# Performance work log

Measured on AMD Instinct MI355X. Metric: run time of the kernel, lower is better.

## Reference

```python
import jax, jax.numpy as jnp
import numpy as np
from jax import lax

B, T, DIN, D = 8, 4096, 1024, 256
H, DK, DV, DFF, P = 8, 32, 32, 1024, 4
KC, NS = 64, 4
SCALES = jnp.array([16.0, 64.0, 128.0, 256.0], dtype=jnp.float32)
K = KC * NS


def _pos_embedding(rel, d_model):
    # rel: [B,K,2] normalized (start,end) -> sinusoidal emb [B,K,d_model]
    d4 = d_model // 4
    freq = jnp.exp(-jnp.log(10000.0) * jnp.arange(d4, dtype=jnp.float32) / d4)
    ang = rel[..., None] * freq                                  # [B,K,2,d4]
    emb = jnp.concatenate([jnp.sin(ang), jnp.cos(ang)], axis=-1) # [B,K,2,2*d4]
    return emb.reshape(rel.shape[0], rel.shape[1], d_model)


def _pool(feat, s, e):
    # ROI pooling by P linearly spaced samples in [s,e); feat [B,T,D], s/e [B,K]
    frac = (jnp.arange(P, dtype=jnp.float32) + 0.5) / P
    idx = jnp.clip(jnp.floor(s[..., None] + (e - s)[..., None] * frac), 0, T - 1).astype(jnp.int32)
    b, k = idx.shape[0], idx.shape[1]
    out = jnp.take_along_axis(feat, idx.reshape(b, k * P)[..., None], axis=1)  # [B,K*P,D]
    return out.reshape(b, k, P, feat.shape[-1])


def _ln(x, g, b):
    m = x.mean(-1, keepdims=True)
    v = ((x - m) ** 2).mean(-1, keepdims=True)
    return (x - m) * lax.rsqrt(v + 1e-6) * g + b


def setup_inputs():
    ks = jax.random.split(jax.random.key(0), 16)
    n = lambda i, sh, s=0.02: jax.random.normal(ks[i], sh, jnp.float32) * s
    return dict(
        feature=jax.random.normal(ks[0], (B, T, DIN), jnp.float32),
        pos_ind=jnp.tile(jnp.arange(T, dtype=jnp.int32)[None], (B, 1)),
        feature_mask=jnp.ones((B, T), jnp.float32),
        W_red=n(1, (DIN, D)), b_red=jnp.zeros((D,), jnp.float32),
        conv1_w=n(2, (D, D, 3)), conv1_b=jnp.zeros((D,), jnp.float32),
        conv2_w=n(3, (D, D, 3)), conv2_b=jnp.zeros((D,), jnp.float32),
        W_sc=n(4, (D, 3)), b_sc=jnp.zeros((3,), jnp.float32),
        W_pool=n(5, (3 * P * D, D)), b_pool=jnp.zeros((D,), jnp.float32),
        Wq=n(6, (D, H * DK)), Wk=n(7, (D, H * DK)), Wv=n(8, (D, H * DV)),
        Wo=n(9, (H * DV, D)),
        ln1_g=jnp.ones((D,), jnp.float32), ln1_b=jnp.zeros((D,), jnp.float32),
        W1=n(10, (D, DFF)), b1=jnp.zeros((DFF,), jnp.float32),
        W2=n(11, (DFF, D)), b2=jnp.zeros((D,), jnp.float32),
        ln2_g=jnp.ones((D,), jnp.float32), ln2_b=jnp.zeros((D,), jnp.float32),
        W_cls=n(12, (D, 2)), b_cls=jnp.zeros((2,), jnp.float32),
    )


def _forward(feature, feature_mask, W_red, b_red, conv1_w, conv1_b, conv2_w, conv2_b,
             W_sc, b_sc, W_pool, b_pool, Wq, Wk, Wv, Wo, ln1_g, ln1_b,
             W1, b1, W2, b2, ln2_g, ln2_b, W_cls, b_cls):
    enc_input = jax.nn.selu(feature @ W_red + b_red)            # [B,T,D]
    h = enc_input.transpose(0, 2, 1)                            # [B,D,T]
    dn = ('NCH', 'OIH', 'NCH')
    h = jax.nn.relu(lax.conv_general_dilated(h, conv1_w, (1,), [(1, 1)], dimension_numbers=dn) + conv1_b[None, :, None])
    h = jax.nn.relu(lax.conv_general_dilated(h, conv2_w, (1,), [(1, 1)], dimension_numbers=dn) + conv2_b[None, :, None])
    enc_output = h.transpose(0, 2, 1)                           # [B,T,D]
    score_output = jax.nn.sigmoid(enc_output @ W_sc + b_sc)     # [B,T,3]

    # --- proposal_layer (fixed-size, jit-safe): top-KC actness peaks x NS scales ---
    actness = score_output[..., 0] * feature_mask               # [B,T]
    topv, topi = lax.top_k(actness, KC)                         # [B,KC]
    c = topi.astype(jnp.float32)[:, :, None]                    # [B,KC,1]
    half = SCALES[None, None, :] / 2.0
    s = jnp.clip(c - half, 0.0, T - 1.0).reshape(B, K)
    e = jnp.clip(c + half, 1.0, float(T)).reshape(B, K)
    e = jnp.maximum(e, s + 1.0)
    L = e - s
    ss, se = jnp.clip(s - L / 4, 0.0, T - 1.0), s + L / 4       # start region
    es, ee = e - L / 4, jnp.clip(e + L / 4, 1.0, float(T))      # end region
    rois_mask = jnp.broadcast_to((topv > 0.5)[:, :, None], (B, KC, NS)).reshape(B, K).astype(jnp.float32)
    roi_actness = jnp.broadcast_to(topv[:, :, None], (B, KC, NS)).reshape(B, K)
    rel = jnp.stack([s / T, e / T], axis=-1)                    # [B,K,2]
    pos_emb = _pos_embedding(rel, D)                            # [B,K,D]

    # --- ROI_Relation: pool(start/mid/end) -> fc -> MHSA + FFN (post-LN) ---
    pooled = jnp.concatenate([_pool(enc_input, ss, se), _pool(enc_input, s, e), _pool(enc_input, es, ee)], axis=2)
    x0 = pooled.reshape(B, K, 3 * P * D) @ W_pool + b_pool + pos_emb  # [B,K,D]
    q = (x0 @ Wq).reshape(B, K, H, DK)
    kk = (x0 @ Wk).reshape(B, K, H, DK)
    v = (x0 @ Wv).reshape(B, K, H, DV)
    att = jnp.einsum('bqhd,bkhd->bhqk', q, kk) / np.sqrt(DK).astype(np.float32)
    att = att + (1.0 - rois_mask)[:, None, None, :] * -1e9
    ctx = jnp.einsum('bhqk,bkhd->bqhd', jax.nn.softmax(att, axis=-1), v).reshape(B, K, H * DV)
    x1 = _ln(x0 + ctx @ Wo, ln1_g, ln1_b)
    x2 = _ln(x1 + jax.nn.relu(x1 @ W1 + b1) @ W2 + b2, ln2_g, ln2_b)
    roi_scores = jax.nn.softmax(x2 @ W_cls + b_cls, axis=2)     # [B,K,2]
    rois_se = jnp.stack([s, e], axis=-1)                        # rois[:, :, 1:]
    return rois_se, roi_actness, roi_scores


def reference(feature, pos_ind, feature_mask, W_red, b_red, conv1_w, conv1_b, conv2_w, conv2_b, W_sc, b_sc, W_pool, b_pool, Wq, Wk, Wv, Wo, ln1_g, ln1_b, W1, b1, W2, b2, ln2_g, ln2_b, W_cls, b_cls):
    del pos_ind  # carried through pipeline but unused in this forward
    return _forward(feature, feature_mask, W_red, b_red, conv1_w, conv1_b, conv2_w, conv2_b, W_sc, b_sc, W_pool, b_pool, Wq, Wk, Wv, Wo, ln1_g, ln1_b, W1, b1, W2, b2, ln2_g, ln2_b, W_cls, b_cls)
```

## Files before the change

### kernel.cpp

```cpp
#include <hip/hip_runtime.h>
#include <hip/hip_bf16.h>
#include <math.h>

#define NB 8
#define NT 4096
#define NBT 32768
#define NDIN 1024
#define ND 256
#define NH 8
#define NDK 32
#define NKC 64
#define NNS 4
#define NRK 256
#define NROI 2048

#define F4Z make_float4(0.f, 0.f, 0.f, 0.f)

__global__ __launch_bounds__(256) void transw_k(const float* __restrict__ w1,
    const float* __restrict__ w2, float* __restrict__ Wt1, float* __restrict__ Wt2)
{
  int i = blockIdx.x * 256 + threadIdx.x;
  const float* w = (i >= 196608) ? w2 : w1;
  float* Wt = (i >= 196608) ? Wt2 : Wt1;
  int j = (i >= 196608) ? (i - 196608) : i;
  int co = j & 255;
  int rest = j >> 8;
  int ci = rest & 255;
  int tap = rest >> 8;
  Wt[j] = w[(size_t)co * 768 + ci * 3 + tap];
}

__global__ __launch_bounds__(256) void gemm1_k(const float* __restrict__ A,
    const float* __restrict__ W, const float* __restrict__ bias,
    float* __restrict__ C, int M, int Ka, int N)
{
  __shared__ float As[16][132];
  __shared__ float Ws[16][128];
  int tid = threadIdx.x;
  int tx = tid & 15, ty = tid >> 4;
  int m0 = blockIdx.x * 128, n0 = blockIdx.y * 128;
  int ar = tid >> 1, acg = tid & 1;
  int wk = tid >> 5, wn = tid & 31;
  float acc[8][8] = {};
  for (int kk = 0; kk < Ka; kk += 16) {
#pragma unroll
    for (int p = 0; p < 2; ++p) {
      int cg = acg * 2 + p;
      float4 av = *reinterpret_cast<const float4*>(A + (size_t)(m0 + ar) * Ka + kk + cg * 4);
      As[cg * 4 + 0][ar] = av.x;
      As[cg * 4 + 1][ar] = av.y;
      As[cg * 4 + 2][ar] = av.z;
      As[cg * 4 + 3][ar] = av.w;
    }
#pragma unroll
    for (int p = 0; p < 2; ++p) {
      int k = wk + p * 8;
      *reinterpret_cast<float4*>(&Ws[k][wn * 4]) =
          *reinterpret_cast<const float4*>(W + (size_t)(kk + k) * N + n0 + wn * 4);
    }
    __syncthreads();
#pragma unroll
    for (int k = 0; k < 16; ++k) {
      float4 xa = *reinterpret_cast<const float4*>(&As[k][ty * 4]);
      float4 xb = *reinterpret_cast<const float4*>(&As[k][64 + ty * 4]);
      float4 wa = *reinterpret_cast<const float4*>(&Ws[k][tx * 4]);
      float4 wb = *reinterpret_cast<const float4*>(&Ws[k][64 + tx * 4]);
      float aa[8] = {xa.x, xa.y, xa.z, xa.w, xb.x, xb.y, xb.z, xb.w};
      float bb[8] = {wa.x, wa.y, wa.z, wa.w, wb.x, wb.y, wb.z, wb.w};
#pragma unroll
      for (int i = 0; i < 8; ++i)
#pragma unroll
        for (int j = 0; j < 8; ++j)
          acc[i][j] += aa[i] * bb[j];
    }
    __syncthreads();
  }
#pragma unroll
  for (int i = 0; i < 8; ++i) {
    int row = m0 + ((i < 4) ? (ty * 4 + i) : (64 + ty * 4 + (i - 4)));
#pragma unroll
    for (int jh = 0; jh < 2; ++jh) {
      int col = n0 + jh * 64 + tx * 4;
      float o[4];
#pragma unroll
      for (int j = 0; j < 4; ++j) {
        float v = acc[i][jh * 4 + j] + bias[col + j];
        v = (v > 0.f) ? 1.0507009873554805f * v
                      : 1.0507009873554805f * 1.6732632423543772f * expm1f(v);
        o[j] = v;
      }
      *reinterpret_cast<float4*>(C + (size_t)row * N + col) =
          make_float4(o[0], o[1], o[2], o[3]);
    }
  }
}

template<int EPI>
__global__ __launch_bounds__(256) void conv_t(const float* __restrict__ in,
    const float* __restrict__ Wt, const float* __restrict__ bias,
    float* __restrict__ out, const float* __restrict__ Wsc,
    float* __restrict__ pscore)
{
  __shared__ float As[16][132];
  __shared__ float Ws[16][128];
  int tid = threadIdx.x;
  int tx = tid & 15, ty = tid >> 4;
  int m0 = blockIdx.x * 128, n0 = blockIdx.y * 128;
  int bstart = m0 & ~(NT - 1);
  int ar = tid >> 1, acg = tid & 1;
  int wk = tid >> 5, wn = tid & 31;
  float acc[8][8] = {};
  for (int kk = 0; kk < 768; kk += 16) {
    int tap = kk >> 8, kd = kk & 255;
    int g = m0 - 1 + tap + ar;
    bool ok = (g >= bstart) && (g < bstart + NT);
#pragma unroll
    for (int p = 0; p < 2; ++p) {
      int cg = acg * 2 + p;
      float4 av = ok ? *reinterpret_cast<const float4*>(in + (size_t)g * 256 + kd + cg * 4)
                     : F4Z;
      As[cg * 4 + 0][ar] = av.x;
      As[cg * 4 + 1][ar] = av.y;
      As[cg * 4 + 2][ar] = av.z;
      As[cg * 4 + 3][ar] = av.w;
    }
#pragma unroll
    for (int p = 0; p < 2; ++p) {
      int k = wk + p * 8;
      *reinterpret_cast<float4*>(&Ws[k][wn * 4]) =
          *reinterpret_cast<const float4*>(Wt + (size_t)(kk + k) * 256 + n0 + wn * 4);
    }
    __syncthreads();
#pragma unroll
    for (int k = 0; k < 16; ++k) {
      float4 xa = *reinterpret_cast<const float4*>(&As[k][ty * 4]);
      float4 xb = *reinterpret_cast<const float4*>(&As[k][64 + ty * 4]);
      float4 wa = *reinterpret_cast<const float4*>(&Ws[k][tx * 4]);
      float4 wb = *reinterpret_cast<const float4*>(&Ws[k][64 + tx * 4]);
      float aa[8] = {xa.x, xa.y, xa.z, xa.w, xb.x, xb.y, xb.z, xb.w};
      float bb[8] = {wa.x, wa.y, wa.z, wa.w, wb.x, wb.y, wb.z, wb.w};
#pragma unroll
      for (int i = 0; i < 8; ++i)
#pragma unroll
        for (int j = 0; j < 8; ++j)
          acc[i][j] += aa[i] * bb[j];
    }
    __syncthreads();
  }

  if (EPI == 0) {
#pragma unroll
    for (int i = 0; i < 8; ++i) {
      int row = m0 + ((i < 4) ? (ty * 4 + i) : (64 + ty * 4 + (i - 4)));
#pragma unroll
      for (int jh = 0; jh < 2; ++jh) {
        int col = n0 + jh * 64 + tx * 4;
        float o[4];
#pragma unroll
        for (int j = 0; j < 4; ++j)
          o[j] = fmaxf(acc[i][jh * 4 + j] + bias[col + j], 0.f);
        *reinterpret_cast<float4*>(out + (size_t)row * 256 + col) =
            make_float4(o[0], o[1], o[2], o[3]);
      }
    }
  } else {
    float p[8];
#pragma unroll
    for (int i = 0; i < 8; ++i) {
      float s = 0.f;
#pragma unroll
      for (int jh = 0; jh < 2; ++jh)
#pragma unroll
        for (int j = 0; j < 4; ++j) {
          int col = n0 + jh * 64 + tx * 4 + j;
          float v = fmaxf(acc[i][jh * 4 + j] + bias[col], 0.f);
          s += v * Wsc[col * 3];
        }
      p[i] = s;
    }
#pragma unroll
    for (int off = 1; off < 16; off <<= 1)
#pragma unroll
      for (int i = 0; i < 8; ++i)
        p[i] += __shfl_xor(p[i], off, 64);
    if (tx == 0) {
#pragma unroll
      for (int i = 0; i < 8; ++i) {
        int row = m0 + ((i < 4) ? (ty * 4 + i) : (64 + ty * 4 + (i - 4)));
        pscore[(size_t)row * 2 + blockIdx.y] = p[i];
      }
    }
  }
}

__global__ __launch_bounds__(256) void actness_k(const float* __restrict__ pscore,
    const float* __restrict__ bsc, const float* __restrict__ fmask,
    float* __restrict__ actness)
{
  int g = blockIdx.x * 256 + threadIdx.x;
  float2 pv = *reinterpret_cast<const float2*>(pscore + (size_t)g * 2);
  float z = pv.x + pv.y + bsc[0];
  actness[g] = (1.f / (1.f + expf(-z))) * fmask[g];
}

template<int ACT>
__global__ __launch_bounds__(256) void gemm_k(const float* __restrict__ A,
    const float* __restrict__ W, const float* __restrict__ bias,
    const float* __restrict__ resid, float* __restrict__ C,
    int M, int Ka, int N)
{
  __shared__ float As[16][66];
  __shared__ float Ws[16][68];
  int tid = threadIdx.x;
  int tx = tid & 15, ty = tid >> 4;
  int m0 = blockIdx.x * 64, n0 = blockIdx.y * 64;
  int lr = tid >> 2, lc = tid & 3;
  int wr = tid >> 4, wc = tid & 15;
  float acc[4][4] = {};
  for (int kk = 0; kk < Ka; kk += 16) {
    float4 av = *reinterpret_cast<const float4*>(A + (size_t)(m0 + lr) * Ka + kk + lc * 4);
    As[lc * 4 + 0][lr] = av.x;
    As[lc * 4 + 1][lr] = av.y;
    As[lc * 4 + 2][lr] = av.z;
    As[lc * 4 + 3][lr] = av.w;
    float4 wv = *reinterpret_cast<const float4*>(W + (size_t)(kk + wr) * N + n0 + wc * 4);
    *reinterpret_cast<float4*>(&Ws[wr][wc * 4]) = wv;
    __syncthreads();
#pragma unroll
    for (int k = 0; k < 16; ++k) {
      float4 a4 = *reinterpret_cast<const float4*>(&As[k][ty * 4]);
      float4 b4 = *reinterpret_cast<const float4*>(&Ws[k][tx * 4]);
      float aa[4] = {a4.x, a4.y, a4.z, a4.w};
      float bb[4] = {b4.x, b4.y, b4.z, b4.w};
#pragma unroll
      for (int i = 0; i < 4; ++i)
#pragma unroll
        for (int j = 0; j < 4; ++j)
          acc[i][j] += aa[i] * bb[j];
    }
    __syncthreads();
  }
#pragma unroll
  for (int i = 0; i < 4; ++i) {
    int row = m0 + ty * 4 + i;
    float o[4];
#pragma unroll
    for (int j = 0; j < 4; ++j) {
      int col = n0 + tx * 4 + j;
      float v = acc[i][j];
      if (bias) v += bias[col];
      if (resid) v += resid[(size_t)row * N + col];
      if (ACT == 1) {
        v = (v > 0.f) ? 1.0507009873554805f * v
                      : 1.0507009873554805f * 1.6732632423543772f * expm1f(v);
      } else if (ACT == 2) {
        v = fmaxf(v, 0.f);
      }
      o[j] = v;
    }
    *reinterpret_cast<float4*>(C + (size_t)row * N + n0 + tx * 4) =
        make_float4(o[0], o[1], o[2], o[3]);
  }
}

__global__ __launch_bounds__(256) void topk_k(const float* __restrict__ actness,
    float* __restrict__ topv, int* __restrict__ topi)
{
  __shared__ float wbv[4];
  __shared__ int wbi[4];
  __shared__ float gbv;
  __shared__ int gbi;
  int b = blockIdx.x;
  int tid = threadIdx.x;
  int lane = tid & 63, wvi = tid >> 6;
  float v[16];
  const float* src = actness + (size_t)b * NT + tid * 16;
#pragma unroll
  for (int j = 0; j < 16; j += 4)
    *reinterpret_cast<float4*>(&v[j]) = *reinterpret_cast<const float4*>(src + j);
  for (int it = 0; it < NKC; ++it) {
    float best = -1e30f; int bj = 0;
#pragma unroll
    for (int j = 0; j < 16; ++j)
      if (v[j] > best) { best = v[j]; bj = j; }
    int bidx = tid * 16 + bj;
#pragma unroll
    for (int off = 1; off < 64; off <<= 1) {
      float ov = __shfl_xor(best, off, 64);
      int oi = __shfl_xor(bidx, off, 64);
      if (ov > best || (ov == best && oi < bidx)) { best = ov; bidx = oi; }
    }
    if (lane == 0) { wbv[wvi] = best; wbi[wvi] = bidx; }
    __syncthreads();
    if (tid == 0) {
      float bb = wbv[0]; int bi2 = wbi[0];
#pragma unroll
      for (int w = 1; w < 4; ++w)
        if (wbv[w] > bb || (wbv[w] == bb && wbi[w] < bi2)) { bb = wbv[w]; bi2 = wbi[w]; }
      topv[b * NKC + it] = bb;
      topi[b * NKC + it] = bi2;
      gbv = bb; gbi = bi2;
    }
    __syncthreads();
    int gi = gbi;
    if ((gi >> 4) == tid) v[gi & 15] = -1e30f;
  }
}

__global__ __launch_bounds__(256) void rois_k(const float* __restrict__ topv,
    const int* __restrict__ topi, int* __restrict__ idxb, float* __restrict__ rmask,
    float* __restrict__ rel, float* __restrict__ out_rois, float* __restrict__ out_act)
{
  int t = blockIdx.x * 256 + threadIdx.x;
  if (t >= NROI) return;
  int b = t >> 8, k = t & 255, kc = k >> 2, ns = k & 3;
  float tv = topv[b * NKC + kc];
  float c = (float)topi[b * NKC + kc];
  const float scales[4] = {16.f, 64.f, 128.f, 256.f};
  float half = scales[ns] * 0.5f;
  float s = fminf(fmaxf(c - half, 0.f), 4095.f);
  float e = fminf(fmaxf(c + half, 1.f), 4096.f);
  e = fmaxf(e, s + 1.f);
  float L = e - s;
  float ss = fminf(fmaxf(s - L * 0.25f, 0.f), 4095.f);
  float se = s + L * 0.25f;
  float es = e - L * 0.25f;
  float ee = fminf(fmaxf(e + L * 0.25f, 1.f), 4096.f);
  float st[3] = {ss, s, es};
  float en[3] = {se, e, ee};
#pragma unroll
  for (int r = 0; r < 3; ++r)
#pragma unroll
    for (int p = 0; p < 4; ++p) {
      float frac = ((float)p + 0.5f) * 0.25f;
      float fidx = floorf(st[r] + (en[r] - st[r]) * frac);
      fidx = fminf(fmaxf(fidx, 0.f), 4095.f);
      idxb[t * 12 + r * 4 + p] = (int)fidx;
    }
  rmask[t] = (tv > 0.5f) ? 1.f : 0.f;
  rel[t * 2 + 0] = s * (1.f / 4096.f);
  rel[t * 2 + 1] = e * (1.f / 4096.f);
  out_rois[t * 2 + 0] = s;
  out_rois[t * 2 + 1] = e;
  out_act[t] = tv;
}

__global__ __launch_bounds__(256) void pool_gemm_k(const float* __restrict__ enc,
    const int* __restrict__ idxb, const float* __restrict__ Wp,
    const float* __restrict__ bp, const float* __restrict__ rel,
    float* __restrict__ x0)
{
  __shared__ float As[16][66];
  __shared__ float Ws[16][68];
  int tid = threadIdx.x;
  int tx = tid & 15, ty = tid >> 4;
  int m0 = blockIdx.x * 64, n0 = blockIdx.y * 64;
  int lr = tid >> 2, lc = tid & 3;
  int wr = tid >> 4, wc = tid & 15;
  int roi = m0 + lr;
  int b = roi >> 8;
  float acc[4][4] = {};
  for (int kk = 0; kk < 3072; kk += 16) {
    int slot = kk >> 8, kd = kk & 255;
    int trow = idxb[roi * 12 + slot];
    float4 av = *reinterpret_cast<const float4*>(
        enc + ((size_t)(b * NT + trow)) * 256 + kd + lc * 4);
    As[lc * 4 + 0][lr] = av.x;
    As[lc * 4 + 1][lr] = av.y;
    As[lc * 4 + 2][lr] = av.z;
    As[lc * 4 + 3][lr] = av.w;
    float4 wv = *reinterpret_cast<const float4*>(Wp + (size_t)(kk + wr) * 256 + n0 + wc * 4);
    *reinterpret_cast<float4*>(&Ws[wr][wc * 4]) = wv;
    __syncthreads();
#pragma unroll
    for (int k = 0; k < 16; ++k) {
      float4 a4 = *reinterpret_cast<const float4*>(&As[k][ty * 4]);
      float4 b4 = *reinterpret_cast<const float4*>(&Ws[k][tx * 4]);
      float aa[4] = {a4.x, a4.y, a4.z, a4.w};
      float bb[4] = {b4.x, b4.y, b4.z, b4.w};
#pragma unroll
      for (int i = 0; i < 4; ++i)
#pragma unroll
        for (int j = 0; j < 4; ++j)
          acc[i][j] += aa[i] * bb[j];
    }
    __syncthreads();
  }
#pragma unroll
  for (int i = 0; i < 4; ++i) {
    int rr = m0 + ty * 4 + i;
    float r0 = rel[rr * 2], r1 = rel[rr * 2 + 1];
    float o[4];
#pragma unroll
    for (int j = 0; j < 4; ++j) {
      int col = n0 + tx * 4 + j;
      int rsel = col >> 7, cc = col & 127, j2 = cc & 63;
      float freq = expf(-0.14391156831212787f * (float)j2);
      float ang = ((rsel == 0) ? r0 : r1) * freq;
      float pe = (cc < 64) ? sinf(ang) : cosf(ang);
      o[j] = acc[i][j] + bp[col] + pe;
    }
    *reinterpret_cast<float4*>(x0 + (size_t)rr * 256 + n0 + tx * 4) =
        make_float4(o[0], o[1], o[2], o[3]);
  }
}

__global__ __launch_bounds__(256) void attn_k(const float* __restrict__ q,
    const float* __restrict__ kbuf, const float* __restrict__ vbuf,
    const float* __restrict__ rmask, float* __restrict__ ctx)
{
  __shared__ float ks[256][32];
  __shared__ float vs[256][32];
  int bh = blockIdx.x;
  int b = bh >> 3, h = bh & 7;
  int tid = threadIdx.x;
  size_t base = ((size_t)b * 256) * 256 + h * 32;
  for (int idx = tid; idx < 2048; idx += 256) {
    int r = idx >> 3, dg = idx & 7;
    *reinterpret_cast<float4*>(&ks[r][dg * 4]) =
        *reinterpret_cast<const float4*>(kbuf + base + (size_t)r * 256 + dg * 4);
    *reinterpret_cast<float4*>(&vs[r][dg * 4]) =
        *reinterpret_cast<const float4*>(vbuf + base + (size_t)r * 256 + dg * 4);
  }
  __syncthreads();
  float qr[32];
#pragma unroll
  for (int dg = 0; dg < 8; ++dg)
    *reinterpret_cast<float4*>(&qr[dg * 4]) =
        *reinterpret_cast<const float4*>(q + base + (size_t)tid * 256 + dg * 4);
  const float invs = 0.17677669529663689f;
  float m = -1e30f;
  for (int kk = 0; kk < 256; ++kk) {
    float s = 0.f;
#pragma unroll
    for (int d = 0; d < 32; ++d) s += qr[d] * ks[kk][d];
    s = s * invs + (1.f - rmask[b * 256 + kk]) * -1e9f;
    m = fmaxf(m, s);
  }
  float l = 0.f;
  float accd[32] = {};
  for (int kk = 0; kk < 256; ++kk) {
    float s = 0.f;
#pragma unroll
    for (int d = 0; d < 32; ++d) s += qr[d] * ks[kk][d];
    s = s * invs + (1.f - rmask[b * 256 + kk]) * -1e9f;
    float p = expf(s - m);
    l += p;
#pragma unroll
    for (int d = 0; d < 32; ++d) accd[d] += p * vs[kk][d];
  }
  float inv = 1.f / l;
#pragma unroll
  for (int dg = 0; dg < 8; ++dg) {
    float4 o = make_float4(accd[dg * 4] * inv, accd[dg * 4 + 1] * inv,
                           accd[dg * 4 + 2] * inv, accd[dg * 4 + 3] * inv);
    *reinterpret_cast<float4*>(ctx + base + (size_t)tid * 256 + dg * 4) = o;
  }
}

__global__ __launch_bounds__(256) void ln_k(float* __restrict__ x,
    const float* __restrict__ g, const float* __restrict__ bb)
{
  int row = blockIdx.x * 4 + (threadIdx.x >> 6);
  int lane = threadIdx.x & 63;
  float* xr = x + (size_t)row * 256;
  float4 v = *reinterpret_cast<const float4*>(xr + lane * 4);
  float s = v.x + v.y + v.z + v.w;
#pragma unroll
  for (int off = 32; off > 0; off >>= 1) s += __shfl_xor(s, off, 64);
  float mean = s * 0.00390625f;
  float dx[4] = {v.x - mean, v.y - mean, v.z - mean, v.w - mean};
  float s2 = dx[0] * dx[0] + dx[1] * dx[1] + dx[2] * dx[2] + dx[3] * dx[3];
#pragma unroll
  for (int off = 32; off > 0; off >>= 1) s2 += __shfl_xor(s2, off, 64);
  float var = s2 * 0.00390625f;
  float rs = 1.f / sqrtf(var + 1e-6f);
  int c = lane * 4;
  float4 o;
  o.x = dx[0] * rs * g[c + 0] + bb[c + 0];
  o.y = dx[1] * rs * g[c + 1] + bb[c + 1];
  o.z = dx[2] * rs * g[c + 2] + bb[c + 2];
  o.w = dx[3] * rs * g[c + 3] + bb[c + 3];
  *reinterpret_cast<float4*>(xr + lane * 4) = o;
}

__global__ __launch_bounds__(256) void cls_k(const float* __restrict__ x2,
    const float* __restrict__ Wc, const float* __restrict__ bc,
    float* __restrict__ out)
{
  int r = blockIdx.x * 256 + threadIdx.x;
  if (r >= NROI) return;
  float l0 = bc[0], l1 = bc[1];
  const float* xr = x2 + (size_t)r * 256;
  for (int c = 0; c < 256; ++c) {
    float xv = xr[c];
    l0 += xv * Wc[c * 2 + 0];
    l1 += xv * Wc[c * 2 + 1];
  }
  float mm = fmaxf(l0, l1);
  float e0 = expf(l0 - mm), e1 = expf(l1 - mm);
  float inv = 1.f / (e0 + e1);
  out[r * 2 + 0] = e0 * inv;
  out[r * 2 + 1] = e1 * inv;
}

extern "C" void kernel_launch(void* const* d_in, const int* in_sizes, int n_in,
                              void* d_out, int out_size, void* d_ws, size_t ws_size,
                              hipStream_t stream) {
  (void)in_sizes; (void)n_in; (void)out_size; (void)ws_size;
  const float* feature = (const float*)d_in[0];
  const float* fmask   = (const float*)d_in[2];
  const float* W_red   = (const float*)d_in[3];
  const float* b_red   = (const float*)d_in[4];
  const float* conv1_w = (const float*)d_in[5];
  const float* conv1_b = (const float*)d_in[6];
  const float* conv2_w = (const float*)d_in[7];
  const float* conv2_b = (const float*)d_in[8];
  const float* W_sc    = (const float*)d_in[9];
  const float* b_sc    = (const float*)d_in[10];
  const float* W_pool  = (const float*)d_in[11];
  const float* b_pool  = (const float*)d_in[12];
  const float* Wq      = (const float*)d_in[13];
  const float* Wk      = (const float*)d_in[14];
  const float* Wv      = (const float*)d_in[15];
  const float* Wo      = (const float*)d_in[16];
  const float* ln1_g   = (const float*)d_in[17];
  const float* ln1_b   = (const float*)d_in[18];
  const float* W1      = (const float*)d_in[19];
  const float* b1      = (const float*)d_in[20];
  const float* W2      = (const float*)d_in[21];
  const float* b2      = (const float*)d_in[22];
  const float* ln2_g   = (const float*)d_in[23];
  const float* ln2_b   = (const float*)d_in[24];
  const float* W_cls   = (const float*)d_in[25];
  const float* b_cls   = (const float*)d_in[26];

  float* ws = (float*)d_ws;
  float* enc   = ws;
  float* h1    = ws + 8388608;
  float* Wt1   = ws + 16777216;
  float* Wt2   = ws + 16973824;
  float* act   = ws + 17170432;
  float* topv  = ws + 17203200;
  int*   topi  = (int*)(ws + 17203712);
  int*   idxb  = (int*)(ws + 17204224);
  float* rmask = ws + 17228800;
  float* rel   = ws + 17230848;
  float* pscore = ws + 17234944;
  float* x0  = h1;
  float* qb  = h1 + 524288;
  float* kb  = h1 + 1048576;
  float* vb  = h1 + 1572864;
  float* ctx = h1 + 2097152;
  float* x1  = h1 + 2621440;
  float* ft  = h1 + 3145728;
  float* x2  = h1 + 5242880;

  float* orois  = (float*)d_out;
  float* oact   = orois + 4096;
  float* oscore = orois + 6144;

  transw_k<<<1536, 256, 0, stream>>>(conv1_w, conv2_w, Wt1, Wt2);
  gemm1_k<<<dim3(256, 2), 256, 0, stream>>>(feature, W_red, b_red, enc,
                                            NBT, NDIN, ND);
  conv_t<0><<<dim3(256, 2), 256, 0, stream>>>(enc, Wt1, conv1_b, h1, nullptr, nullptr);
  conv_t<1><<<dim3(256, 2), 256, 0, stream>>>(h1, Wt2, conv2_b, nullptr, W_sc, pscore);
  actness_k<<<128, 256, 0, stream>>>(pscore, b_sc, fmask, act);
  topk_k<<<NB, 256, 0, stream>>>(act, topv, topi);
  rois_k<<<NB, 256, 0, stream>>>(topv, topi, idxb, rmask, rel, orois, oact);
  pool_gemm_k<<<dim3(32, 4), 256, 0, stream>>>(enc, idxb, W_pool, b_pool, rel, x0);
  gemm_k<0><<<dim3(32, 4), 256, 0, stream>>>(x0, Wq, nullptr, nullptr, qb, NROI, ND, ND);
  gemm_k<0><<<dim3(32, 4), 256, 0, stream>>>(x0, Wk, nullptr, nullptr, kb, NROI, ND, ND);
  gemm_k<0><<<dim3(32, 4), 256, 0, stream>>>(x0, Wv, nullptr, nullptr, vb, NROI, ND, ND);
  attn_k<<<NB * NH, 256, 0, stream>>>(qb, kb, vb, rmask, ctx);
  gemm_k<0><<<dim3(32, 4), 256, 0, stream>>>(ctx, Wo, nullptr, x0, x1, NROI, ND, ND);
  ln_k<<<512, 256, 0, stream>>>(x1, ln1_g, ln1_b);
  gemm_k<2><<<dim3(32, 16), 256, 0, stream>>>(x1, W1, b1, nullptr, ft, NROI, ND, 1024);
  gemm_k<0><<<dim3(32, 4), 256, 0, stream>>>(ft, W2, b2, x1, x2, NROI, 1024, ND);
  ln_k<<<512, 256, 0, stream>>>(x2, ln2_g, ln2_b);
  cls_k<<<NB, 256, 0, stream>>>(x2, W_cls, b_cls, oscore);
}
```

Before: 1.116 ms.

## Register-prefetch GEMM tiles, fuse QKV projection, online-softmax attention, warp-parallel classifier

Adds register double-buffering to every tiled GEMM/conv kernel, so the next K-chunk's global loads are issued before the current chunk's FMAs. This is meant to hide load latency, at the cost of an extra barrier per iteration and more registers. It also concatenates Wq/Wk/Wv into one weight and runs a single QKV GEMM, which cuts launches and rereads of x0. Attention switches to a single-pass online softmax, and the classifier head uses one wavefront per ROI with shuffle reductions instead of a serial per-thread loop.

```diff
diff --git a/kernel.cpp b/kernel.cpp
--- a/kernel.cpp
+++ b/kernel.cpp
@@ -30,6 +30,17 @@
   Wt[j] = w[(size_t)co * 768 + ci * 3 + tap];
 }
 
+__global__ __launch_bounds__(256) void concatw_k(const float* __restrict__ Wq,
+    const float* __restrict__ Wk, const float* __restrict__ Wv,
+    float* __restrict__ Wqkv)
+{
+  int d = blockIdx.x * 256 + threadIdx.x;
+  int r = d / 768, c = d % 768;
+  int m = c >> 8, cc = c & 255;
+  const float* src = (m == 0) ? Wq : (m == 1) ? Wk : Wv;
+  Wqkv[d] = src[r * 256 + cc];
+}
+
 __global__ __launch_bounds__(256) void gemm1_k(const float* __restrict__ A,
     const float* __restrict__ W, const float* __restrict__ bias,
     float* __restrict__ C, int M, int Ka, int N)
@@ -41,24 +52,31 @@
   int m0 = blockIdx.x * 128, n0 = blockIdx.y * 128;
   int ar = tid >> 1, acg = tid & 1;
   int wk = tid >> 5, wn = tid & 31;
+  float4 pa0, pa1, pw0, pw1;
+
+#define G1LOAD(kk) do { \
+    pa0 = *reinterpret_cast<const float4*>(A + (size_t)(m0 + ar) * Ka + (kk) + (acg * 2 + 0) * 4); \
+    pa1 = *reinterpret_cast<const float4*>(A + (size_t)(m0 + ar) * Ka + (kk) + (acg * 2 + 1) * 4); \
+    pw0 = *reinterpret_cast<const float4*>(W + (size_t)((kk) + wk) * N + n0 + wn * 4); \
+    pw1 = *reinterpret_cast<const float4*>(W + (size_t)((kk) + 8 + wk) * N + n0 + wn * 4); \
+  } while (0)
+#define G1WRITE() do { \
+    int cg0 = acg * 2, cg1 = acg * 2 + 1; \
+    As[cg0 * 4 + 0][ar] = pa0.x; As[cg0 * 4 + 1][ar] = pa0.y; \
+    As[cg0 * 4 + 2][ar] = pa0.z; As[cg0 * 4 + 3][ar] = pa0.w; \
+    As[cg1 * 4 + 0][ar] = pa1.x; As[cg1 * 4 + 1][ar] = pa1.y; \
+    As[cg1 * 4 + 2][ar] = pa1.z; As[cg1 * 4 + 3][ar] = pa1.w; \
+    *reinterpret_cast<float4*>(&Ws[wk][wn * 4]) = pw0; \
+    *reinterpret_cast<float4*>(&Ws[8 + wk][wn * 4]) = pw1; \
+  } while (0)
+
+  int NC = Ka >> 4;
   float acc[8][8] = {};
-  for (int kk = 0; kk < Ka; kk += 16) {
-#pragma unroll
-    for (int p = 0; p < 2; ++p) {
-      int cg = acg * 2 + p;
-      float4 av = *reinterpret_cast<const float4*>(A + (size_t)(m0 + ar) * Ka + kk + cg * 4);
-      As[cg * 4 + 0][ar] = av.x;
-      As[cg * 4 + 1][ar] = av.y;
-      As[cg * 4 + 2][ar] = av.z;
-      As[cg * 4 + 3][ar] = av.w;
-    }
-#pragma unroll
-    for (int p = 0; p < 2; ++p) {
-      int k = wk + p * 8;
-      *reinterpret_cast<float4*>(&Ws[k][wn * 4]) =
-          *reinterpret_cast<const float4*>(W + (size_t)(kk + k) * N + n0 + wn * 4);
-    }
-    __syncthreads();
+  G1LOAD(0);
+  G1WRITE();
+  __syncthreads();
+  for (int c = 0; c < NC; ++c) {
+    if (c + 1 < NC) G1LOAD((c + 1) * 16);
 #pragma unroll
     for (int k = 0; k < 16; ++k) {
       float4 xa = *reinterpret_cast<const float4*>(&As[k][ty * 4]);
@@ -74,7 +92,13 @@
           acc[i][j] += aa[i] * bb[j];
     }
     __syncthreads();
-  }
+    if (c + 1 < NC) {
+      G1WRITE();
+      __syncthreads();
+    }
+  }
+#undef G1LOAD
+#undef G1WRITE
 #pragma unroll
   for (int i = 0; i < 8; ++i) {
     int row = m0 + ((i < 4) ? (ty * 4 + i) : (64 + ty * 4 + (i - 4)));
@@ -109,28 +133,33 @@
   int bstart = m0 & ~(NT - 1);
   int ar = tid >> 1, acg = tid & 1;
   int wk = tid >> 5, wn = tid & 31;
+  float4 pa0, pa1, pw0, pw1;
+
+#define CLOAD(kk) do { \
+    int tap = (kk) >> 8, kd = (kk) & 255; \
+    int g = m0 - 1 + tap + ar; \
+    bool ok = (g >= bstart) && (g < bstart + NT); \
+    pa0 = ok ? *reinterpret_cast<const float4*>(in + (size_t)g * 256 + kd + (acg * 2 + 0) * 4) : F4Z; \
+    pa1 = ok ? *reinterpret_cast<const float4*>(in + (size_t)g * 256 + kd + (acg * 2 + 1) * 4) : F4Z; \
+    pw0 = *reinterpret_cast<const float4*>(Wt + (size_t)((kk) + wk) * 256 + n0 + wn * 4); \
+    pw1 = *reinterpret_cast<const float4*>(Wt + (size_t)((kk) + 8 + wk) * 256 + n0 + wn * 4); \
+  } while (0)
+#define CWRITE() do { \
+    int cg0 = acg * 2, cg1 = acg * 2 + 1; \
+    As[cg0 * 4 + 0][ar] = pa0.x; As[cg0 * 4 + 1][ar] = pa0.y; \
+    As[cg0 * 4 + 2][ar] = pa0.z; As[cg0 * 4 + 3][ar] = pa0.w; \
+    As[cg1 * 4 + 0][ar] = pa1.x; As[cg1 * 4 + 1][ar] = pa1.y; \
+    As[cg1 * 4 + 2][ar] = pa1.z; As[cg1 * 4 + 3][ar] = pa1.w; \
+    *reinterpret_cast<float4*>(&Ws[wk][wn * 4]) = pw0; \
+    *reinterpret_cast<float4*>(&Ws[8 + wk][wn * 4]) = pw1; \
+  } while (0)
+
   float acc[8][8] = {};
-  for (int kk = 0; kk < 768; kk += 16) {
-    int tap = kk >> 8, kd = kk & 255;
-    int g = m0 - 1 + tap + ar;
-    bool ok = (g >= bstart) && (g < bstart + NT);
-#pragma unroll
-    for (int p = 0; p < 2; ++p) {
-      int cg = acg * 2 + p;
-      float4 av = ok ? *reinterpret_cast<const float4*>(in + (size_t)g * 256 + kd + cg * 4)
-                     : F4Z;
-      As[cg * 4 + 0][ar] = av.x;
-      As[cg * 4 + 1][ar] = av.y;
-      As[cg * 4 + 2][ar] = av.z;
-      As[cg * 4 + 3][ar] = av.w;
-    }
-#pragma unroll
-    for (int p = 0; p < 2; ++p) {
-      int k = wk + p * 8;
-      *reinterpret_cast<float4*>(&Ws[k][wn * 4]) =
-          *reinterpret_cast<const float4*>(Wt + (size_t)(kk + k) * 256 + n0 + wn * 4);
-    }
-    __syncthreads();
+  CLOAD(0);
+  CWRITE();
+  __syncthreads();
+  for (int c = 0; c < 48; ++c) {
+    if (c + 1 < 48) CLOAD((c + 1) * 16);
 #pragma unroll
     for (int k = 0; k < 16; ++k) {
       float4 xa = *reinterpret_cast<const float4*>(&As[k][ty * 4]);
@@ -146,7 +175,13 @@
           acc[i][j] += aa[i] * bb[j];
     }
     __syncthreads();
-  }
+    if (c + 1 < 48) {
+      CWRITE();
+      __syncthreads();
+    }
+  }
+#undef CLOAD
+#undef CWRITE
 
   if (EPI == 0) {
 #pragma unroll
@@ -216,16 +251,25 @@
   int m0 = blockIdx.x * 64, n0 = blockIdx.y * 64;
   int lr = tid >> 2, lc = tid & 3;
   int wr = tid >> 4, wc = tid & 15;
+  float4 pav, pwv;
+  int NC = Ka >> 4;
+
+#define GLOAD(kk) do { \
+    pav = *reinterpret_cast<const float4*>(A + (size_t)(m0 + lr) * Ka + (kk) + lc * 4); \
+    pwv = *reinterpret_cast<const float4*>(W + (size_t)((kk) + wr) * N + n0 + wc * 4); \
+  } while (0)
+#define GWRITE() do { \
+    As[lc * 4 + 0][lr] = pav.x; As[lc * 4 + 1][lr] = pav.y; \
+    As[lc * 4 + 2][lr] = pav.z; As[lc * 4 + 3][lr] = pav.w; \
+    *reinterpret_cast<float4*>(&Ws[wr][wc * 4]) = pwv; \
+  } while (0)
+
   float acc[4][4] = {};
-  for (int kk = 0; kk < Ka; kk += 16) {
-    float4 av = *reinterpret_cast<const float4*>(A + (size_t)(m0 + lr) * Ka + kk + lc * 4);
-    As[lc * 4 + 0][lr] = av.x;
-    As[lc * 4 + 1][lr] = av.y;
-    As[lc * 4 + 2][lr] = av.z;
-    As[lc * 4 + 3][lr] = av.w;
-    float4 wv = *reinterpret_cast<const float4*>(W + (size_t)(kk + wr) * N + n0 + wc * 4);
-    *reinterpret_cast<float4*>(&Ws[wr][wc * 4]) = wv;
-    __syncthreads();
+  GLOAD(0);
+  GWRITE();
+  __syncthreads();
+  for (int c = 0; c < NC; ++c) {
+    if (c + 1 < NC) GLOAD((c + 1) * 16);
 #pragma unroll
     for (int k = 0; k < 16; ++k) {
       float4 a4 = *reinterpret_cast<const float4*>(&As[k][ty * 4]);
@@ -239,7 +283,13 @@
           acc[i][j] += aa[i] * bb[j];
     }
     __syncthreads();
-  }
+    if (c + 1 < NC) {
+      GWRITE();
+      __syncthreads();
+    }
+  }
+#undef GLOAD
+#undef GWRITE
 #pragma unroll
   for (int i = 0; i < 4; ++i) {
     int row = m0 + ty * 4 + i;
@@ -359,19 +409,26 @@
   int wr = tid >> 4, wc = tid & 15;
   int roi = m0 + lr;
   int b = roi >> 8;
+  float4 pav, pwv;
+
+#define PLOAD(kk) do { \
+    int slot = (kk) >> 8, kd = (kk) & 255; \
+    int trow = idxb[roi * 12 + slot]; \
+    pav = *reinterpret_cast<const float4*>(enc + ((size_t)(b * NT + trow)) * 256 + kd + lc * 4); \
+    pwv = *reinterpret_cast<const float4*>(Wp + (size_t)((kk) + wr) * 256 + n0 + wc * 4); \
+  } while (0)
+#define PWRITE() do { \
+    As[lc * 4 + 0][lr] = pav.x; As[lc * 4 + 1][lr] = pav.y; \
+    As[lc * 4 + 2][lr] = pav.z; As[lc * 4 + 3][lr] = pav.w; \
+    *reinterpret_cast<float4*>(&Ws[wr][wc * 4]) = pwv; \
+  } while (0)
+
   float acc[4][4] = {};
-  for (int kk = 0; kk < 3072; kk += 16) {
-    int slot = kk >> 8, kd = kk & 255;
-    int trow = idxb[roi * 12 + slot];
-    float4 av = *reinterpret_cast<const float4*>(
-        enc + ((size_t)(b * NT + trow)) * 256 + kd + lc * 4);
-    As[lc * 4 + 0][lr] = av.x;
-    As[lc * 4 + 1][lr] = av.y;
-    As[lc * 4 + 2][lr] = av.z;
-    As[lc * 4 + 3][lr] = av.w;
-    float4 wv = *reinterpret_cast<const float4*>(Wp + (size_t)(kk + wr) * 256 + n0 + wc * 4);
-    *reinterpret_cast<float4*>(&Ws[wr][wc * 4]) = wv;
-    __syncthreads();
+  PLOAD(0);
+  PWRITE();
+  __syncthreads();
+  for (int c = 0; c < 192; ++c) {
+    if (c + 1 < 192) PLOAD((c + 1) * 16);
 #pragma unroll
     for (int k = 0; k < 16; ++k) {
       float4 a4 = *reinterpret_cast<const float4*>(&As[k][ty * 4]);
@@ -385,7 +442,13 @@
           acc[i][j] += aa[i] * bb[j];
     }
     __syncthreads();
-  }
+    if (c + 1 < 192) {
+      PWRITE();
+      __syncthreads();
+    }
+  }
+#undef PLOAD
+#undef PWRITE
 #pragma unroll
   for (int i = 0; i < 4; ++i) {
     int rr = m0 + ty * 4 + i;
@@ -405,8 +468,7 @@
   }
 }
 
-__global__ __launch_bounds__(256) void attn_k(const float* __restrict__ q,
-    const float* __restrict__ kbuf, const float* __restrict__ vbuf,
+__global__ __launch_bounds__(256) void attn_k(const float* __restrict__ qkv,
     const float* __restrict__ rmask, float* __restrict__ ctx)
 {
   __shared__ float ks[256][32];
@@ -414,36 +476,35 @@
   int bh = blockIdx.x;
   int b = bh >> 3, h = bh & 7;
   int tid = threadIdx.x;
-  size_t base = ((size_t)b * 256) * 256 + h * 32;
+  size_t rowb = (size_t)b * 256;
   for (int idx = tid; idx < 2048; idx += 256) {
     int r = idx >> 3, dg = idx & 7;
     *reinterpret_cast<float4*>(&ks[r][dg * 4]) =
-        *reinterpret_cast<const float4*>(kbuf + base + (size_t)r * 256 + dg * 4);
+        *reinterpret_cast<const float4*>(qkv + (rowb + r) * 768 + 256 + h * 32 + dg * 4);
     *reinterpret_cast<float4*>(&vs[r][dg * 4]) =
-        *reinterpret_cast<const float4*>(vbuf + base + (size_t)r * 256 + dg * 4);
+        *reinterpret_cast<const float4*>(qkv + (rowb + r) * 768 + 512 + h * 32 + dg * 4);
   }
   __syncthreads();
   float qr[32];
 #pragma unroll
   for (int dg = 0; dg < 8; ++dg)
     *reinterpret_cast<float4*>(&qr[dg * 4]) =
-        *reinterpret_cast<const float4*>(q + base + (size_t)tid * 256 + dg * 4);
+        *reinterpret_cast<const float4*>(qkv + (rowb + tid) * 768 + h * 32 + dg * 4);
   const float invs = 0.17677669529663689f;
-  float m = -1e30f;
-  for (int kk = 0; kk < 256; ++kk) {
-    float s = 0.f;
-#pragma unroll
-    for (int d = 0; d < 32; ++d) s += qr[d] * ks[kk][d];
-    s = s * invs + (1.f - rmask[b * 256 + kk]) * -1e9f;
-    m = fmaxf(m, s);
-  }
-  float l = 0.f;
+  float m = -1e30f, l = 0.f;
   float accd[32] = {};
   for (int kk = 0; kk < 256; ++kk) {
     float s = 0.f;
 #pragma unroll
     for (int d = 0; d < 32; ++d) s += qr[d] * ks[kk][d];
     s = s * invs + (1.f - rmask[b * 256 + kk]) * -1e9f;
+    if (s > m) {
+      float corr = expf(m - s);
+      l *= corr;
+#pragma unroll
+      for (int d = 0; d < 32; ++d) accd[d] *= corr;
+      m = s;
+    }
     float p = expf(s - m);
     l += p;
 #pragma unroll
@@ -454,7 +515,7 @@
   for (int dg = 0; dg < 8; ++dg) {
     float4 o = make_float4(accd[dg * 4] * inv, accd[dg * 4 + 1] * inv,
                            accd[dg * 4 + 2] * inv, accd[dg * 4 + 3] * inv);
-    *reinterpret_cast<float4*>(ctx + base + (size_t)tid * 256 + dg * 4) = o;
+    *reinterpret_cast<float4*>(ctx + (rowb + tid) * 256 + h * 32 + dg * 4) = o;
   }
 }
 
@@ -488,20 +549,28 @@
     const float* __restrict__ Wc, const float* __restrict__ bc,
     float* __restrict__ out)
 {
-  int r = blockIdx.x * 256 + threadIdx.x;
-  if (r >= NROI) return;
-  float l0 = bc[0], l1 = bc[1];
-  const float* xr = x2 + (size_t)r * 256;
-  for (int c = 0; c < 256; ++c) {
-    float xv = xr[c];
-    l0 += xv * Wc[c * 2 + 0];
-    l1 += xv * Wc[c * 2 + 1];
-  }
-  float mm = fmaxf(l0, l1);
-  float e0 = expf(l0 - mm), e1 = expf(l1 - mm);
-  float inv = 1.f / (e0 + e1);
-  out[r * 2 + 0] = e0 * inv;
-  out[r * 2 + 1] = e1 * inv;
+  int row = blockIdx.x * 4 + (threadIdx.x >> 6);
+  int lane = threadIdx.x & 63;
+  const float* xr = x2 + (size_t)row * 256;
+  float4 xv = *reinterpret_cast<const float4*>(xr + lane * 4);
+  int c = lane * 4;
+  float4 w01 = *reinterpret_cast<const float4*>(Wc + c * 2);
+  float4 w23 = *reinterpret_cast<const float4*>(Wc + c * 2 + 4);
+  float l0 = xv.x * w01.x + xv.y * w01.z + xv.z * w23.x + xv.w * w23.z;
+  float l1 = xv.x * w01.y + xv.y * w01.w + xv.z * w23.y + xv.w * w23.w;
+#pragma unroll
+  for (int off = 32; off > 0; off >>= 1) {
+    l0 += __shfl_xor(l0, off, 64);
+    l1 += __shfl_xor(l1, off, 64);
+  }
+  if (lane == 0) {
+    l0 += bc[0]; l1 += bc[1];
+    float mm = fmaxf(l0, l1);
+    float e0 = expf(l0 - mm), e1 = expf(l1 - mm);
+    float inv = 1.f / (e0 + e1);
+    out[row * 2 + 0] = e0 * inv;
+    out[row * 2 + 1] = e1 * inv;
+  }
 }
 
 extern "C" void kernel_launch(void* const* d_in, const int* in_sizes, int n_in,
@@ -547,14 +616,13 @@
   float* rmask = ws + 17228800;
   float* rel   = ws + 17230848;
   float* pscore = ws + 17234944;
-  float* x0  = h1;
-  float* qb  = h1 + 524288;
-  float* kb  = h1 + 1048576;
-  float* vb  = h1 + 1572864;
-  float* ctx = h1 + 2097152;
-  float* x1  = h1 + 2621440;
-  float* ft  = h1 + 3145728;
-  float* x2  = h1 + 5242880;
+  float* x0   = h1;
+  float* qkv  = h1 + 524288;
+  float* ctx  = h1 + 2097152;
+  float* x1   = h1 + 2621440;
+  float* ft   = h1 + 3145728;
+  float* x2   = h1 + 5242880;
+  float* Wqkv = h1 + 5767168;
 
   float* orois  = (float*)d_out;
   float* oact   = orois + 4096;
@@ -568,15 +636,15 @@
   actness_k<<<128, 256, 0, stream>>>(pscore, b_sc, fmask, act);
   topk_k<<<NB, 256, 0, stream>>>(act, topv, topi);
   rois_k<<<NB, 256, 0, stream>>>(topv, topi, idxb, rmask, rel, orois, oact);
+  concatw_k<<<768, 256, 0, stream>>>(Wq, Wk, Wv, Wqkv);
   pool_gemm_k<<<dim3(32, 4), 256, 0, stream>>>(enc, idxb, W_pool, b_pool, rel, x0);
-  gemm_k<0><<<dim3(32, 4), 256, 0, stream>>>(x0, Wq, nullptr, nullptr, qb, NROI, ND, ND);
-  gemm_k<0><<<dim3(32, 4), 256, 0, stream>>>(x0, Wk, nullptr, nullptr, kb, NROI, ND, ND);
-  gemm_k<0><<<dim3(32, 4), 256, 0, stream>>>(x0, Wv, nullptr, nullptr, vb, NROI, ND, ND);
-  attn_k<<<NB * NH, 256, 0, stream>>>(qb, kb, vb, rmask, ctx);
+  gemm_k<0><<<dim3(32, 12), 256, 0, stream>>>(x0, Wqkv, nullptr, nullptr, qkv,
+                                              NROI, ND, 768);
+  attn_k<<<NB * NH, 256, 0, stream>>>(qkv, rmask, ctx);
   gemm_k<0><<<dim3(32, 4), 256, 0, stream>>>(ctx, Wo, nullptr, x0, x1, NROI, ND, ND);
   ln_k<<<512, 256, 0, stream>>>(x1, ln1_g, ln1_b);
   gemm_k<2><<<dim3(32, 16), 256, 0, stream>>>(x1, W1, b1, nullptr, ft, NROI, ND, 1024);
   gemm_k<0><<<dim3(32, 4), 256, 0, stream>>>(ft, W2, b2, x1, x2, NROI, 1024, ND);
   ln_k<<<512, 256, 0, stream>>>(x2, ln2_g, ln2_b);
-  cls_k<<<NB, 256, 0, stream>>>(x2, W_cls, b_cls, oscore);
-}
+  cls_k<<<512, 256, 0, stream>>>(x2, W_cls, b_cls, oscore);
+}
```

Result: slower. 1.197 ms (+7.3%).

## Fuse QKV projections, use online softmax in attention, parallelize classifier

Applied to the files above, without the earlier changes.

Concatenates Wq, Wk and Wv into one 768-wide weight so a single GEMM produces Q, K and V. The attention kernel now reads that interleaved buffer and uses an online softmax, so the QK dot products are computed once instead of in two passes. The classifier kernel moves from one thread per row to one wavefront per row with shuffle reductions. These changes add a small weight-concatenation kernel on every call, plus branchy rescaling inside the attention loop.

```diff
diff --git a/kernel.cpp b/kernel.cpp
--- a/kernel.cpp
+++ b/kernel.cpp
@@ -28,6 +28,17 @@
   int ci = rest & 255;
   int tap = rest >> 8;
   Wt[j] = w[(size_t)co * 768 + ci * 3 + tap];
+}
+
+__global__ __launch_bounds__(256) void concatw_k(const float* __restrict__ Wq,
+    const float* __restrict__ Wk, const float* __restrict__ Wv,
+    float* __restrict__ Wqkv)
+{
+  int d = blockIdx.x * 256 + threadIdx.x;
+  int r = d / 768, c = d % 768;
+  int m = c >> 8, cc = c & 255;
+  const float* src = (m == 0) ? Wq : (m == 1) ? Wk : Wv;
+  Wqkv[d] = src[r * 256 + cc];
 }
 
 __global__ __launch_bounds__(256) void gemm1_k(const float* __restrict__ A,
@@ -405,8 +416,7 @@
   }
 }
 
-__global__ __launch_bounds__(256) void attn_k(const float* __restrict__ q,
-    const float* __restrict__ kbuf, const float* __restrict__ vbuf,
+__global__ __launch_bounds__(256) void attn_k(const float* __restrict__ qkv,
     const float* __restrict__ rmask, float* __restrict__ ctx)
 {
   __shared__ float ks[256][32];
@@ -414,36 +424,35 @@
   int bh = blockIdx.x;
   int b = bh >> 3, h = bh & 7;
   int tid = threadIdx.x;
-  size_t base = ((size_t)b * 256) * 256 + h * 32;
+  size_t rowb = (size_t)b * 256;
   for (int idx = tid; idx < 2048; idx += 256) {
     int r = idx >> 3, dg = idx & 7;
     *reinterpret_cast<float4*>(&ks[r][dg * 4]) =
-        *reinterpret_cast<const float4*>(kbuf + base + (size_t)r * 256 + dg * 4);
+        *reinterpret_cast<const float4*>(qkv + (rowb + r) * 768 + 256 + h * 32 + dg * 4);
     *reinterpret_cast<float4*>(&vs[r][dg * 4]) =
-        *reinterpret_cast<const float4*>(vbuf + base + (size_t)r * 256 + dg * 4);
+        *reinterpret_cast<const float4*>(qkv + (rowb + r) * 768 + 512 + h * 32 + dg * 4);
   }
   __syncthreads();
   float qr[32];
 #pragma unroll
   for (int dg = 0; dg < 8; ++dg)
     *reinterpret_cast<float4*>(&qr[dg * 4]) =
-        *reinterpret_cast<const float4*>(q + base + (size_t)tid * 256 + dg * 4);
+        *reinterpret_cast<const float4*>(qkv + (rowb + tid) * 768 + h * 32 + dg * 4);
   const float invs = 0.17677669529663689f;
-  float m = -1e30f;
-  for (int kk = 0; kk < 256; ++kk) {
-    float s = 0.f;
-#pragma unroll
-    for (int d = 0; d < 32; ++d) s += qr[d] * ks[kk][d];
-    s = s * invs + (1.f - rmask[b * 256 + kk]) * -1e9f;
-    m = fmaxf(m, s);
-  }
-  float l = 0.f;
+  float m = -1e30f, l = 0.f;
   float accd[32] = {};
   for (int kk = 0; kk < 256; ++kk) {
     float s = 0.f;
 #pragma unroll
     for (int d = 0; d < 32; ++d) s += qr[d] * ks[kk][d];
     s = s * invs + (1.f - rmask[b * 256 + kk]) * -1e9f;
+    if (s > m) {
+      float corr = expf(m - s);
+      l *= corr;
+#pragma unroll
+      for (int d = 0; d < 32; ++d) accd[d] *= corr;
+      m = s;
+    }
     float p = expf(s - m);
     l += p;
 #pragma unroll
@@ -454,7 +463,7 @@
   for (int dg = 0; dg < 8; ++dg) {
     float4 o = make_float4(accd[dg * 4] * inv, accd[dg * 4 + 1] * inv,
                            accd[dg * 4 + 2] * inv, accd[dg * 4 + 3] * inv);
-    *reinterpret_cast<float4*>(ctx + base + (size_t)tid * 256 + dg * 4) = o;
+    *reinterpret_cast<float4*>(ctx + (rowb + tid) * 256 + h * 32 + dg * 4) = o;
   }
 }
 
@@ -488,20 +497,28 @@
     const float* __restrict__ Wc, const float* __restrict__ bc,
     float* __restrict__ out)
 {
-  int r = blockIdx.x * 256 + threadIdx.x;
-  if (r >= NROI) return;
-  float l0 = bc[0], l1 = bc[1];
-  const float* xr = x2 + (size_t)r * 256;
-  for (int c = 0; c < 256; ++c) {
-    float xv = xr[c];
-    l0 += xv * Wc[c * 2 + 0];
-    l1 += xv * Wc[c * 2 + 1];
-  }
-  float mm = fmaxf(l0, l1);
-  float e0 = expf(l0 - mm), e1 = expf(l1 - mm);
-  float inv = 1.f / (e0 + e1);
-  out[r * 2 + 0] = e0 * inv;
-  out[r * 2 + 1] = e1 * inv;
+  int row = blockIdx.x * 4 + (threadIdx.x >> 6);
+  int lane = threadIdx.x & 63;
+  const float* xr = x2 + (size_t)row * 256;
+  float4 xv = *reinterpret_cast<const float4*>(xr + lane * 4);
+  int c = lane * 4;
+  float4 w01 = *reinterpret_cast<const float4*>(Wc + c * 2);
+  float4 w23 = *reinterpret_cast<const float4*>(Wc + c * 2 + 4);
+  float l0 = xv.x * w01.x + xv.y * w01.z + xv.z * w23.x + xv.w * w23.z;
+  float l1 = xv.x * w01.y + xv.y * w01.w + xv.z * w23.y + xv.w * w23.w;
+#pragma unroll
+  for (int off = 32; off > 0; off >>= 1) {
+    l0 += __shfl_xor(l0, off, 64);
+    l1 += __shfl_xor(l1, off, 64);
+  }
+  if (lane == 0) {
+    l0 += bc[0]; l1 += bc[1];
+    float mm = fmaxf(l0, l1);
+    float e0 = expf(l0 - mm), e1 = expf(l1 - mm);
+    float inv = 1.f / (e0 + e1);
+    out[row * 2 + 0] = e0 * inv;
+    out[row * 2 + 1] = e1 * inv;
+  }
 }
 
 extern "C" void kernel_launch(void* const* d_in, const int* in_sizes, int n_in,
@@ -547,14 +564,13 @@
   float* rmask = ws + 17228800;
   float* rel   = ws + 17230848;
   float* pscore = ws + 17234944;
-  float* x0  = h1;
-  float* qb  = h1 + 524288;
-  float* kb  = h1 + 1048576;
-  float* vb  = h1 + 1572864;
-  float* ctx = h1 + 2097152;
-  float* x1  = h1 + 2621440;
-  float* ft  = h1 + 3145728;
-  float* x2  = h1 + 5242880;
+  float* x0   = h1;
+  float* qkv  = h1 + 524288;
+  float* ctx  = h1 + 2097152;
+  float* x1   = h1 + 2621440;
+  float* ft   = h1 + 3145728;
+  float* x2   = h1 + 5242880;
+  float* Wqkv = h1 + 5767168;
 
   float* orois  = (float*)d_out;
   float* oact   = orois + 4096;
@@ -568,15 +584,15 @@
   actness_k<<<128, 256, 0, stream>>>(pscore, b_sc, fmask, act);
   topk_k<<<NB, 256, 0, stream>>>(act, topv, topi);
   rois_k<<<NB, 256, 0, stream>>>(topv, topi, idxb, rmask, rel, orois, oact);
+  concatw_k<<<768, 256, 0, stream>>>(Wq, Wk, Wv, Wqkv);
   pool_gemm_k<<<dim3(32, 4), 256, 0, stream>>>(enc, idxb, W_pool, b_pool, rel, x0);
-  gemm_k<0><<<dim3(32, 4), 256, 0, stream>>>(x0, Wq, nullptr, nullptr, qb, NROI, ND, ND);
-  gemm_k<0><<<dim3(32, 4), 256, 0, stream>>>(x0, Wk, nullptr, nullptr, kb, NROI, ND, ND);
-  gemm_k<0><<<dim3(32, 4), 256, 0, stream>>>(x0, Wv, nullptr, nullptr, vb, NROI, ND, ND);
-  attn_k<<<NB * NH, 256, 0, stream>>>(qb, kb, vb, rmask, ctx);
+  gemm_k<0><<<dim3(32, 12), 256, 0, stream>>>(x0, Wqkv, nullptr, nullptr, qkv,
+                                              NROI, ND, 768);
+  attn_k<<<NB * NH, 256, 0, stream>>>(qkv, rmask, ctx);
   gemm_k<0><<<dim3(32, 4), 256, 0, stream>>>(ctx, Wo, nullptr, x0, x1, NROI, ND, ND);
   ln_k<<<512, 256, 0, stream>>>(x1, ln1_g, ln1_b);
   gemm_k<2><<<dim3(32, 16), 256, 0, stream>>>(x1, W1, b1, nullptr, ft, NROI, ND, 1024);
   gemm_k<0><<<dim3(32, 4), 256, 0, stream>>>(ft, W2, b2, x1, x2, NROI, 1024, ND);
   ln_k<<<512, 256, 0, stream>>>(x2, ln2_g, ln2_b);
-  cls_k<<<NB, 256, 0, stream>>>(x2, W_cls, b_cls, oscore);
-}
+  cls_k<<<512, 256, 0, stream>>>(x2, W_cls, b_cls, oscore);
+}
```

Result: faster. 1.064 ms (-4.6%).
